# Performance work log

Measured on AMD Instinct MI355X. Metric: run time of the kernel, lower is better.

Reference implementation:

```python
import jax, jax.numpy as jnp
import numpy as np

IN_DIM, HID, E, N = 1024, 2048, 8, 16384

def setup_inputs() -> dict:
    key = jax.random.key(0)
    ks = jax.random.split(key, 12)
    s_in = 1.0 / np.sqrt(IN_DIM)
    s_h = 1.0 / np.sqrt(HID)
    return {
        "x": jax.random.normal(ks[0], (N, IN_DIM), dtype=jnp.float32),
        "enc_W": jax.random.uniform(ks[1], (IN_DIM, HID), jnp.float32, -s_in, s_in),
        "enc_b": jax.random.uniform(ks[2], (HID,), jnp.float32, -s_in, s_in),
        "gate_W": jax.random.uniform(ks[3], (HID, E), jnp.float32, -s_h, s_h),
        "expert_W": jax.random.uniform(ks[4], (E, HID, HID), jnp.float32, -s_h, s_h),
        "expert_b": jax.random.uniform(ks[5], (E, HID), jnp.float32, -s_h, s_h),
        "res_W": jax.random.uniform(ks[6], (HID, HID), jnp.float32, -s_h, s_h),
        "res_b": jax.random.uniform(ks[7], (HID,), jnp.float32, -s_h, s_h),
        "coef_W": jax.random.uniform(ks[8], (HID, 2), jnp.float32, -s_h, s_h),
        "coef_b": jax.random.uniform(ks[9], (2,), jnp.float32, -s_h, s_h),
        "dec_W": jax.random.uniform(ks[10], (HID, IN_DIM), jnp.float32, -s_h, s_h),
        "dec_b": jax.random.uniform(ks[11], (IN_DIM,), jnp.float32, -s_h, s_h),
    }

def reference(x, enc_W, enc_b, gate_W, expert_W, expert_b, res_W, res_b, coef_W, coef_b, dec_W, dec_b):
    # Encode: Linear + ReLU -> h [N, HID]
    h = jax.nn.relu(x @ enc_W + enc_b)
    # Top-1 gating (softmax probs, argmax expert, combine weight = chosen prob)
    probs = jax.nn.softmax(h @ gate_W, axis=-1)          # [N, E]
    idx = jnp.argmax(probs, axis=-1)                     # [N]
    gate = jnp.max(probs, axis=-1, keepdims=True)        # [N, 1]
    # Dense dispatch: run every expert, select via one-hot combine
    y_all = jnp.einsum('nd,edh->neh', h, expert_W) + expert_b  # [N, E, HID]
    onehot = jax.nn.one_hot(idx, y_all.shape[1], dtype=h.dtype)
    moe_out = jnp.einsum('neh,ne->nh', y_all, onehot) * gate   # [N, HID]
    # Residual expert + learned 2-way blending coefficient
    res = h @ res_W + res_b
    coef = jax.nn.softmax(h @ coef_W + coef_b, axis=-1)        # [N, 2]
    out = moe_out * coef[:, 0:1] + res * coef[:, 1:2]
    # Decode
    return out @ dec_W + dec_b
```

## Files before the change

kernel.cpp:

```cpp
#include <hip/hip_runtime.h>


#define N_TOK 16384
#define IN_DIM 1024
#define HID 2048
#define NEXP 8
#define TAU 8.0e-3f

typedef __bf16 bf16_t;
typedef __bf16 bf16x8 __attribute__((ext_vector_type(8)));
typedef __bf16 bf16x4v __attribute__((ext_vector_type(4)));
typedef float f32x4 __attribute__((ext_vector_type(4)));
typedef unsigned short ushort_t;

#define CLAMP1E4(v) fmaxf(fminf((v), 1.0e4f), -1.0e4f)

#define ASYNC16(gp, lp)                                                        \
  __builtin_amdgcn_global_load_lds(                                            \
      (const __attribute__((address_space(1))) void*)(gp),                     \
      (__attribute__((address_space(3))) void*)(lp), 16, 0, 0)

static __device__ inline ushort_t b2u(bf16_t v) {
  union { bf16_t b; ushort_t u; } x; x.b = v; return x.u;
}

__global__ __launch_bounds__(256) void fill_bf16(bf16_t* __restrict__ p,
                                                 float v, int n) {
  const int i = blockIdx.x * 256 + threadIdx.x;
  if (i < n) p[i] = (bf16_t)v;
}

__global__ __launch_bounds__(256) void detect_dtype(
    const ushort_t* __restrict__ xr, int* __restrict__ flag) {
  __shared__ int s_bad;
  if (threadIdx.x == 0) s_bad = 0;
  __syncthreads();
  int bad = 0;
  for (int i = threadIdx.x; i < 4096; i += 256) {
    const int e = (xr[i] >> 7) & 0xFF;
    if (e >= 0xC0) bad = 1;
  }
  if (__any(bad) && (threadIdx.x & 63) == 0) atomicOr(&s_bad, 1);
  __syncthreads();
  if (threadIdx.x == 0) *flag = s_bad;
}

__global__ __launch_bounds__(256) void cvt_to_bf16_x4(
    const void* __restrict__ src, bf16_t* __restrict__ dst, int n4,
    const int* __restrict__ flagp) {
  const int f = *flagp;
  const int i = blockIdx.x * 256 + threadIdx.x;
  if (i >= n4) return;
  bf16x4v o;
  if (f) {
    const f32x4 v = ((const f32x4*)src)[i];
    o[0] = (bf16_t)v[0]; o[1] = (bf16_t)v[1];
    o[2] = (bf16_t)v[2]; o[3] = (bf16_t)v[3];
  } else {
    o = ((const bf16x4v*)src)[i];
  }
  ((bf16x4v*)dst)[i] = o;
}

__global__ __launch_bounds__(256) void cvt_small(
    const void* __restrict__ encB, const void* __restrict__ expB,
    const void* __restrict__ resB, const void* __restrict__ decB,
    const void* __restrict__ coefB, const void* __restrict__ gateW,
    const void* __restrict__ coefW, float* __restrict__ encBf,
    float* __restrict__ expBf, float* __restrict__ resBf,
    float* __restrict__ decBf, float* __restrict__ coefBf,
    bf16_t* __restrict__ gWb, bf16_t* __restrict__ cWb,
    const int* __restrict__ flagp) {
  const int f = *flagp;
  const int i = blockIdx.x * 256 + threadIdx.x;
  const int seg = blockIdx.y;
  const void* src;
  int n;
  switch (seg) {
    case 0: src = encB;  n = HID; break;
    case 1: src = expB;  n = NEXP * HID; break;
    case 2: src = resB;  n = HID; break;
    case 3: src = decB;  n = IN_DIM; break;
    case 4: src = coefB; n = 2; break;
    case 5: src = gateW; n = HID * 8; break;
    default: src = coefW; n = HID * 2; break;
  }
  if (i >= n) return;
  const float v = f ? ((const float*)src)[i] : (float)((const bf16_t*)src)[i];
  switch (seg) {
    case 0: encBf[i] = v; break;
    case 1: expBf[i] = v; break;
    case 2: resBf[i] = v; break;
    case 3: decBf[i] = v; break;
    case 4: coefBf[i] = v; break;
    case 5: gWb[i] = (bf16_t)v; break;
    default: cWb[i] = (bf16_t)v; break;
  }
}

__global__ __launch_bounds__(256) void transpose_cvt(
    const void* __restrict__ src0, ushort_t* __restrict__ dst, int R, int C,
    size_t elem_off, const int* __restrict__ flagp, size_t src_zstride,
    size_t dst_zstride) {
  __shared__ ushort_t t[32][33];
  const int f = *flagp;
  const size_t eoff = elem_off + (size_t)blockIdx.z * src_zstride;
  dst += (size_t)blockIdx.z * dst_zstride;
  const int c0 = blockIdx.x * 32, r0 = blockIdx.y * 32;
  const int tx = threadIdx.x, ty = threadIdx.y;
  if (f) {
    const float* s = (const float*)src0 + eoff;
#pragma unroll
    for (int i = 0; i < 4; ++i)
      t[ty + i * 8][tx] =
          b2u((bf16_t)s[(size_t)(r0 + ty + i * 8) * C + c0 + tx]);
  } else {
    const ushort_t* s = (const ushort_t*)src0 + eoff;
#pragma unroll
    for (int i = 0; i < 4; ++i)
      t[ty + i * 8][tx] = s[(size_t)(r0 + ty + i * 8) * C + c0 + tx];
  }
  __syncthreads();
#pragma unroll
  for (int i = 0; i < 4; ++i)
    dst[(size_t)(c0 + ty + i * 8) * R + r0 + tx] = t[tx][ty + i * 8];
}


__global__ __launch_bounds__(256) void enc_gemm(
    const bf16_t* __restrict__ A, const bf16_t* __restrict__ Bt,
    const float* __restrict__ bias, bf16_t* __restrict__ H) {
  __shared__ bf16_t As[128 * 64];
  __shared__ bf16_t Bs[128 * 64];

  const int tid = threadIdx.x, lane = tid & 63, w = tid >> 6;
  const int wr = w >> 1, wc = w & 1, quad = lane >> 4, l16 = lane & 15;
  const int m0 = blockIdx.x * 128, n0 = blockIdx.y * 128;
  const char* Ab = (const char*)A;
  const char* Bb = (const char*)Bt;
  const size_t lda = (size_t)IN_DIM * 2;

  const f32x4 fz = {0.f, 0.f, 0.f, 0.f};
  f32x4 acc[4][4];
#pragma unroll
  for (int i = 0; i < 4; ++i)
#pragma unroll
    for (int j = 0; j < 4; ++j) acc[i][j] = fz;

  size_t aoff[4], boff[4];
  int cb[4];
#pragma unroll
  for (int c = 0; c < 4; ++c) {
    cb[c] = (w * 4 + c) * 1024;
    const int o = cb[c] + lane * 16;
    const int row = o >> 7;
    const int kb = (o & 127) ^ ((row & 7) << 4);
    aoff[c] = (size_t)(m0 + row) * lda + kb;
    boff[c] = (size_t)(n0 + row) * lda + kb;
  }
  const int sw = (l16 & 7) << 3;

  for (int kt = 0; kt < IN_DIM / 64; ++kt) {
    __syncthreads();
#pragma unroll
    for (int c = 0; c < 4; ++c) {
      ASYNC16(Ab + aoff[c] + (size_t)kt * 128, (char*)As + cb[c]);
      ASYNC16(Bb + boff[c] + (size_t)kt * 128, (char*)Bs + cb[c]);
    }
    __syncthreads();

#pragma unroll
    for (int ks = 0; ks < 2; ++ks) {
      const int co = (ks * 32 + quad * 8) ^ sw;
      bf16x8 af[4], bfr[4];
#pragma unroll
      for (int i = 0; i < 4; ++i)
        af[i] = *(const bf16x8*)&As[(wr * 64 + i * 16 + l16) * 64 + co];
#pragma unroll
      for (int j = 0; j < 4; ++j)
        bfr[j] = *(const bf16x8*)&Bs[(wc * 64 + j * 16 + l16) * 64 + co];
#pragma unroll
      for (int i = 0; i < 4; ++i)
#pragma unroll
        for (int j = 0; j < 4; ++j)
          acc[i][j] = __builtin_amdgcn_mfma_f32_16x16x32_bf16(
              af[i], bfr[j], acc[i][j], 0, 0, 0);
    }
  }

  float bj[4];
  int colj[4];
#pragma unroll
  for (int j = 0; j < 4; ++j) {
    colj[j] = n0 + wc * 64 + j * 16 + l16;
    bj[j] = bias[colj[j]];
  }

#pragma unroll
  for (int i = 0; i < 4; ++i) {
#pragma unroll
    for (int r = 0; r < 4; ++r) {
      const int row = m0 + wr * 64 + i * 16 + quad * 4 + r;
#pragma unroll
      for (int j = 0; j < 4; ++j) {
        const float v = fminf(fmaxf(acc[i][j][r] + bj[j], 0.f), 1.0e4f);
        H[(size_t)row * HID + colj[j]] = (bf16_t)v;
      }
    }
  }
}

__global__ __launch_bounds__(256) void gate_from_h(
    const bf16_t* __restrict__ H, const bf16_t* __restrict__ gW,
    const bf16_t* __restrict__ cW, const float* __restrict__ coefBf,
    float* __restrict__ s0g, float* __restrict__ s1g, float* __restrict__ c0g,
    int* __restrict__ eidx, int* __restrict__ ambig, int* __restrict__ acnt,
    int* __restrict__ cnt) {
  const int tid = threadIdx.x, lane = tid & 63, w = tid >> 6;
  const int r0 = blockIdx.x * 16 + w * 4;

  float acc[4][10];
#pragma unroll
  for (int g = 0; g < 4; ++g)
#pragma unroll
    for (int o = 0; o < 10; ++o) acc[g][o] = 0.f;

#pragma unroll
  for (int it = 0; it < HID / 512; ++it) {
    const int h0 = it * 512 + lane * 8;
    bf16x8 hv[4];
#pragma unroll
    for (int g = 0; g < 4; ++g)
      hv[g] = *(const bf16x8*)(H + (size_t)(r0 + g) * HID + h0);
    const bf16_t* gp = gW + (size_t)h0 * 8;
    const bf16_t* cp = cW + (size_t)h0 * 2;
    bf16x8 cc0 = *(const bf16x8*)(cp);
    bf16x8 cc1 = *(const bf16x8*)(cp + 8);
#pragma unroll
    for (int k = 0; k < 8; ++k) {
      const bf16x8 gk = *(const bf16x8*)(gp + k * 8);
      const float ck0 = (k < 4) ? (float)cc0[(k & 3) * 2]
                                : (float)cc1[(k & 3) * 2];
      const float ck1 = (k < 4) ? (float)cc0[(k & 3) * 2 + 1]
                                : (float)cc1[(k & 3) * 2 + 1];
#pragma unroll
      for (int g = 0; g < 4; ++g) {
        const float v = (float)hv[g][k];
#pragma unroll
        for (int o = 0; o < 8; ++o) acc[g][o] += v * (float)gk[o];
        acc[g][8] += v * ck0;
        acc[g][9] += v * ck1;
      }
    }
  }

#pragma unroll
  for (int m = 1; m < 64; m <<= 1)
#pragma unroll
    for (int g = 0; g < 4; ++g)
#pragma unroll
      for (int o = 0; o < 10; ++o) acc[g][o] += __shfl_xor(acc[g][o], m);

  if (lane == 0) {
#pragma unroll
    for (int g = 0; g < 4; ++g) {
      const int r = r0 + g;
      float lv[8];
#pragma unroll
      for (int e = 0; e < 8; ++e) lv[e] = acc[g][e];
      float mx = lv[0];
      int idx = 0;
#pragma unroll
      for (int e = 1; e < 8; ++e)
        if (lv[e] > mx) { mx = lv[e]; idx = e; }
      float s2 = -1.0e30f;
#pragma unroll
      for (int e = 0; e < 8; ++e)
        if (e != idx) s2 = fmaxf(s2, lv[e]);
      float s = 0.f;
#pragma unroll
      for (int e = 0; e < 8; ++e) s += expf(lv[e] - mx);
      const float gate = 1.f / s;
      const float c0 = acc[g][8] + coefBf[0], c1 = acc[g][9] + coefBf[1];
      const float cm = fmaxf(c0, c1);
      const float e0 = expf(c0 - cm), e1 = expf(c1 - cm);
      const float inv = 1.f / (e0 + e1);
      const float p0 = e0 * inv;
      c0g[r] = p0;
      s1g[r] = e1 * inv;
      s0g[r] = gate * p0;
      eidx[r] = idx;
      atomicAdd(&cnt[idx], 1);
      if (mx - s2 < TAU) {
        const int p = atomicAdd(acnt, 1);
        ambig[p] = r;
      }
    }
  }
}

__global__ __launch_bounds__(256) void rescue_partial(
    const void* __restrict__ xraw, const void* __restrict__ encWraw,
    const float* __restrict__ encBf, const void* __restrict__ gateWraw,
    const int* __restrict__ flagp, const int* __restrict__ ambig,
    const int* __restrict__ acnt, double* __restrict__ pglg) {
  const int i = blockIdx.x;
  if (i >= *acnt) return;
  const int s = blockIdx.y;
  const int r = ambig[i];
  const int f = *flagp;
  const int tid = threadIdx.x;
  const int j = s * 256 + tid;

  __shared__ float xs[IN_DIM];
  if (f) {
    const float* xp = (const float*)xraw + (size_t)r * IN_DIM;
    for (int k = tid; k < IN_DIM; k += 256) xs[k] = xp[k];
  } else {
    const bf16_t* xp = (const bf16_t*)xraw + (size_t)r * IN_DIM;
    for (int k = tid; k < IN_DIM; k += 256) xs[k] = (float)xp[k];
  }
  __syncthreads();

  double hacc = 0.0;
  if (f) {
    const float* W = (const float*)encWraw + j;
    for (int k0 = 0; k0 < IN_DIM; k0 += 16) {
      float wv[16];
#pragma unroll
      for (int kk = 0; kk < 16; ++kk) wv[kk] = W[(size_t)(k0 + kk) * HID];
#pragma unroll
      for (int kk = 0; kk < 16; ++kk)
        hacc += (double)xs[k0 + kk] * (double)wv[kk];
    }
  } else {
    const bf16_t* W = (const bf16_t*)encWraw + j;
    for (int k0 = 0; k0 < IN_DIM; k0 += 16) {
      float wv[16];
#pragma unroll
      for (int kk = 0; kk < 16; ++kk)
        wv[kk] = (float)W[(size_t)(k0 + kk) * HID];
#pragma unroll
      for (int kk = 0; kk < 16; ++kk)
        hacc += (double)xs[k0 + kk] * (double)wv[kk];
    }
  }

  double lg[8] = {0, 0, 0, 0, 0, 0, 0, 0};
  const double h = hacc + (double)encBf[j];
  if (h > 0.0) {
    if (f) {
      const float* g = (const float*)gateWraw + (size_t)j * 8;
#pragma unroll
      for (int e = 0; e < 8; ++e) lg[e] = h * (double)g[e];
    } else {
      const bf16_t* g = (const bf16_t*)gateWraw + (size_t)j * 8;
#pragma unroll
      for (int e = 0; e < 8; ++e) lg[e] = h * (double)(float)g[e];
    }
  }
#pragma unroll
  for (int m = 1; m < 64; m <<= 1)
#pragma unroll
    for (int e = 0; e < 8; ++e) lg[e] += __shfl_xor(lg[e], m);

  __shared__ double red[4][8];
  const int w = tid >> 6, lane = tid & 63;
  if (lane == 0)
#pragma unroll
    for (int e = 0; e < 8; ++e) red[w][e] = lg[e];
  __syncthreads();
  if (tid == 0) {
#pragma unroll
    for (int e = 0; e < 8; ++e)
      pglg[((size_t)i * 8 + s) * 8 + e] =
          red[0][e] + red[1][e] + red[2][e] + red[3][e];
  }
}

__global__ __launch_bounds__(64) void rescue_final(
    const int* __restrict__ ambig, const int* __restrict__ acnt,
    const float* __restrict__ c0g, const double* __restrict__ pglg,
    float* __restrict__ s0g, int* __restrict__ eidx, int* __restrict__ cnt) {
  const int i = blockIdx.x;
  if (i >= *acnt || threadIdx.x != 0) return;
  const int r = ambig[i];
  double t[8];
#pragma unroll
  for (int e = 0; e < 8; ++e) {
    double a = 0.0;
#pragma unroll
    for (int s = 0; s < 8; ++s) a += pglg[((size_t)i * 8 + s) * 8 + e];
    t[e] = a;
  }
  double m = t[0];
  int idx = 0;
#pragma unroll
  for (int e = 1; e < 8; ++e)
    if (t[e] > m) { m = t[e]; idx = e; }
  double s = 0.0;
#pragma unroll
  for (int e = 0; e < 8; ++e) s += exp(t[e] - m);
  s0g[r] = (float)((1.0 / s) * (double)c0g[r]);
  const int old = eidx[r];
  if (idx != old) {
    atomicSub(&cnt[old], 1);
    atomicAdd(&cnt[idx], 1);
    eidx[r] = idx;
  }
}

__global__ __launch_bounds__(256) void rescue_rows(
    const void* __restrict__ xraw, const void* __restrict__ encWraw,
    const float* __restrict__ encBf, const void* __restrict__ gateWraw,
    const int* __restrict__ flagp, const int* __restrict__ ambig,
    const int* __restrict__ acnt, const float* __restrict__ c0g,
    float* __restrict__ s0g, int* __restrict__ eidx, int* __restrict__ cnt,
    int ioff) {
  const int i = blockIdx.x + ioff;
  if (i >= *acnt) return;
  const int r = ambig[i];
  const int f = *flagp;
  const int tid = threadIdx.x;

  __shared__ float xs[IN_DIM];
  if (f) {
    const float* xp = (const float*)xraw + (size_t)r * IN_DIM;
    for (int k = tid; k < IN_DIM; k += 256) xs[k] = xp[k];
  } else {
    const bf16_t* xp = (const bf16_t*)xraw + (size_t)r * IN_DIM;
    for (int k = tid; k < IN_DIM; k += 256) xs[k] = (float)xp[k];
  }
  __syncthreads();

  double hacc[8] = {0, 0, 0, 0, 0, 0, 0, 0};
  if (f) {
    const float* W = (const float*)encWraw;
    for (int k0 = 0; k0 < IN_DIM; k0 += 8) {
      float wv[8][8];
#pragma unroll
      for (int kk = 0; kk < 8; ++kk) {
        const float* Wr = W + (size_t)(k0 + kk) * HID + tid;
#pragma unroll
        for (int jj = 0; jj < 8; ++jj) wv[kk][jj] = Wr[jj * 256];
      }
#pragma unroll
      for (int kk = 0; kk < 8; ++kk) {
        const double xv = (double)xs[k0 + kk];
#pragma unroll
        for (int jj = 0; jj < 8; ++jj) hacc[jj] += xv * (double)wv[kk][jj];
      }
    }
  } else {
    const bf16_t* W = (const bf16_t*)encWraw;
    for (int k0 = 0; k0 < IN_DIM; k0 += 8) {
      float wv[8][8];
#pragma unroll
      for (int kk = 0; kk < 8; ++kk) {
        const bf16_t* Wr = W + (size_t)(k0 + kk) * HID + tid;
#pragma unroll
        for (int jj = 0; jj < 8; ++jj) wv[kk][jj] = (float)Wr[jj * 256];
      }
#pragma unroll
      for (int kk = 0; kk < 8; ++kk) {
        const double xv = (double)xs[k0 + kk];
#pragma unroll
        for (int jj = 0; jj < 8; ++jj) hacc[jj] += xv * (double)wv[kk][jj];
      }
    }
  }

  double lg[8] = {0, 0, 0, 0, 0, 0, 0, 0};
#pragma unroll
  for (int jj = 0; jj < 8; ++jj) {
    const int j = tid + jj * 256;
    double h = hacc[jj] + (double)encBf[j];
    if (h > 0.0) {
      if (f) {
        const float* g = (const float*)gateWraw + (size_t)j * 8;
#pragma unroll
        for (int e = 0; e < 8; ++e) lg[e] += h * (double)g[e];
      } else {
        const bf16_t* g = (const bf16_t*)gateWraw + (size_t)j * 8;
#pragma unroll
        for (int e = 0; e < 8; ++e) lg[e] += h * (double)(float)g[e];
      }
    }
  }
#pragma unroll
  for (int m = 1; m < 64; m <<= 1)
#pragma unroll
    for (int e = 0; e < 8; ++e) lg[e] += __shfl_xor(lg[e], m);

  __shared__ double red[4][8];
  const int w = tid >> 6, lane = tid & 63;
  if (lane == 0)
#pragma unroll
    for (int e = 0; e < 8; ++e) red[w][e] = lg[e];
  __syncthreads();
  if (tid == 0) {
    double t[8];
#pragma unroll
    for (int e = 0; e < 8; ++e)
      t[e] = red[0][e] + red[1][e] + red[2][e] + red[3][e];
    double m = t[0];
    int idx = 0;
#pragma unroll
    for (int e = 1; e < 8; ++e)
      if (t[e] > m) { m = t[e]; idx = e; }
    double s = 0.0;
#pragma unroll
    for (int e = 0; e < 8; ++e) s += exp(t[e] - m);
    s0g[r] = (float)((1.0 / s) * (double)c0g[r]);
    const int old = eidx[r];
    if (idx != old) {
      atomicSub(&cnt[old], 1);
      atomicAdd(&cnt[idx], 1);
      eidx[r] = idx;
    }
  }
}

__global__ __launch_bounds__(256) void place_rows(
    const int* __restrict__ eidx, const int* __restrict__ cnt,
    int* __restrict__ curs, int* __restrict__ permflat) {
  const int r = blockIdx.x * 256 + threadIdx.x;
  const int e = eidx[r];
  int prefix = 0;
  for (int ee = 0; ee < NEXP; ++ee)
    if (ee < e) prefix += cnt[ee];
  const int pos = atomicAdd(&curs[e], 1);
  permflat[prefix + pos] = r;
}

__global__ __launch_bounds__(256) void gather_rows(
    const bf16_t* __restrict__ H, const int* __restrict__ permflat,
    const float* __restrict__ s0g, const float* __restrict__ s1g,
    bf16_t* __restrict__ Hp, int* __restrict__ rowid,
    float* __restrict__ s0p, float* __restrict__ s1p) {
  const int w = threadIdx.x >> 6, lane = threadIdx.x & 63;
  const int p = blockIdx.x * 4 + w;
  const int r = permflat[p];
  if (lane == 0) {
    rowid[p] = r;
    s0p[p] = s0g[r];
    s1p[p] = s1g[r];
  }
  const bf16x8* src = (const bf16x8*)(H + (size_t)r * HID);
  bf16x8* dst = (bf16x8*)(Hp + (size_t)p * HID);
#pragma unroll
  for (int i = 0; i < 4; ++i) dst[lane + i * 64] = src[lane + i * 64];
}

__global__ __launch_bounds__(256) void expert_gemm_t(
    const bf16_t* __restrict__ Hp, const bf16_t* __restrict__ wTall,
    size_t wstride, const float* __restrict__ expBf,
    const int* __restrict__ cnt, const int* __restrict__ rowid,
    const float* __restrict__ s0p, bf16_t* __restrict__ mid) {
  __shared__ bf16_t As[128 * 64];
  __shared__ bf16_t Bs[128 * 64];
  __shared__ int rows_s[128];
  __shared__ float s0_s[128];

  const int x = blockIdx.x;
  int e = -1, base = 0, nrows = 0;
  {
    int acc = 0, pre = 0;
    for (int ee = 0; ee < NEXP; ++ee) {
      const int ce = cnt[ee];
      const int nt = (ce + 127) >> 7;
      if (x < acc + nt) {
        const int t = x - acc;
        e = ee;
        base = pre + t * 128;
        nrows = ce - t * 128;
        if (nrows > 128) nrows = 128;
        break;
      }
      acc += nt;
      pre += ce;
    }
  }
  if (e < 0) return;

  const int tid = threadIdx.x, lane = tid & 63, w = tid >> 6;
  const int wr = w >> 1, wc = w & 1, quad = lane >> 4, l16 = lane & 15;

  if (tid < 128) {
    int grow = -1;
    float a0 = 0.f;
    if (tid < nrows) {
      grow = rowid[base + tid];
      a0 = s0p[base + tid];
    }
    rows_s[tid] = grow;
    s0_s[tid] = a0;
  }
  __syncthreads();

  const int n0 = blockIdx.y * 128;
  const char* Hb = (const char*)Hp;
  const char* Wb = (const char*)(wTall + (size_t)e * wstride);

  size_t aoff[4], boff[4];
  int cb[4];
#pragma unroll
  for (int c = 0; c < 4; ++c) {
    cb[c] = (w * 4 + c) * 1024;
    const int o = cb[c] + lane * 16;
    const int row = o >> 7;
    const int kb = (o & 127) ^ ((row & 7) << 4);
    int ar = base + row;
    if (ar > N_TOK - 1) ar = N_TOK - 1;
    aoff[c] = (size_t)ar * (HID * 2) + kb;
    boff[c] = (size_t)(n0 + row) * (HID * 2) + kb;
  }
  const int sw = (l16 & 7) << 3;

  const f32x4 fz = {0.f, 0.f, 0.f, 0.f};
  f32x4 acc[4][4];
#pragma unroll
  for (int i = 0; i < 4; ++i)
#pragma unroll
    for (int j = 0; j < 4; ++j) acc[i][j] = fz;

  for (int kt = 0; kt < HID / 64; ++kt) {
    __syncthreads();
#pragma unroll
    for (int c = 0; c < 4; ++c) {
      ASYNC16(Hb + aoff[c] + (size_t)kt * 128, (char*)As + cb[c]);
      ASYNC16(Wb + boff[c] + (size_t)kt * 128, (char*)Bs + cb[c]);
    }
    __syncthreads();

#pragma unroll
    for (int ks = 0; ks < 2; ++ks) {
      const int co = (ks * 32 + quad * 8) ^ sw;
      bf16x8 af[4], bfr[4];
#pragma unroll
      for (int i = 0; i < 4; ++i)
        af[i] = *(const bf16x8*)&As[(wr * 64 + i * 16 + l16) * 64 + co];
#pragma unroll
      for (int j = 0; j < 4; ++j)
        bfr[j] = *(const bf16x8*)&Bs[(wc * 64 + j * 16 + l16) * 64 + co];
#pragma unroll
      for (int i = 0; i < 4; ++i)
#pragma unroll
        for (int j = 0; j < 4; ++j)
          acc[i][j] = __builtin_amdgcn_mfma_f32_16x16x32_bf16(
              af[i], bfr[j], acc[i][j], 0, 0, 0);
    }
  }

  const float* eBe = expBf + (size_t)e * HID;
  float beb[4];
  int colj[4];
#pragma unroll
  for (int j = 0; j < 4; ++j) {
    colj[j] = n0 + wc * 64 + j * 16 + l16;
    beb[j] = eBe[colj[j]];
  }
#pragma unroll
  for (int i = 0; i < 4; ++i) {
#pragma unroll
    for (int r = 0; r < 4; ++r) {
      const int lr = wr * 64 + i * 16 + quad * 4 + r;
      const int grow = rows_s[lr];
      if (grow < 0) continue;
      const float s0 = s0_s[lr];
#pragma unroll
      for (int j = 0; j < 4; ++j) {
        const float v = CLAMP1E4(s0 * (acc[i][j][r] + beb[j]));
        mid[(size_t)grow * HID + colj[j]] = (bf16_t)v;
      }
    }
  }
}

__global__ __launch_bounds__(256) void res_gemm_p(
    const bf16_t* __restrict__ Hp, const bf16_t* __restrict__ Bt,
    const float* __restrict__ rB, const int* __restrict__ rowid,
    const float* __restrict__ s1p, bf16_t* __restrict__ mid) {
  __shared__ bf16_t As[128 * 64];
  __shared__ bf16_t Bs[128 * 64];

  const int tid = threadIdx.x, lane = tid & 63, w = tid >> 6;
  const int wr = w >> 1, wc = w & 1, quad = lane >> 4, l16 = lane & 15;
  const int m0 = blockIdx.x * 128, n0 = blockIdx.y * 128;
  const char* Ab = (const char*)Hp;
  const char* Bb = (const char*)Bt;

  size_t aoff[4], boff[4];
  int cb[4];
#pragma unroll
  for (int c = 0; c < 4; ++c) {
    cb[c] = (w * 4 + c) * 1024;
    const int o = cb[c] + lane * 16;
    const int row = o >> 7;
    const int kb = (o & 127) ^ ((row & 7) << 4);
    aoff[c] = (size_t)(m0 + row) * (HID * 2) + kb;
    boff[c] = (size_t)(n0 + row) * (HID * 2) + kb;
  }
  const int sw = (l16 & 7) << 3;

  const f32x4 fz = {0.f, 0.f, 0.f, 0.f};
  f32x4 acc[4][4];
#pragma unroll
  for (int i = 0; i < 4; ++i)
#pragma unroll
    for (int j = 0; j < 4; ++j) acc[i][j] = fz;

  for (int kt = 0; kt < HID / 64; ++kt) {
    __syncthreads();
#pragma unroll
    for (int c = 0; c < 4; ++c) {
      ASYNC16(Ab + aoff[c] + (size_t)kt * 128, (char*)As + cb[c]);
      ASYNC16(Bb + boff[c] + (size_t)kt * 128, (char*)Bs + cb[c]);
    }
    __syncthreads();

#pragma unroll
    for (int ks = 0; ks < 2; ++ks) {
      const int co = (ks * 32 + quad * 8) ^ sw;
      bf16x8 af[4], bfr[4];
#pragma unroll
      for (int i = 0; i < 4; ++i)
        af[i] = *(const bf16x8*)&As[(wr * 64 + i * 16 + l16) * 64 + co];
#pragma unroll
      for (int j = 0; j < 4; ++j)
        bfr[j] = *(const bf16x8*)&Bs[(wc * 64 + j * 16 + l16) * 64 + co];
#pragma unroll
      for (int i = 0; i < 4; ++i)
#pragma unroll
        for (int j = 0; j < 4; ++j)
          acc[i][j] = __builtin_amdgcn_mfma_f32_16x16x32_bf16(
              af[i], bfr[j], acc[i][j], 0, 0, 0);
    }
  }

  float rbb[4];
  int colj[4];
#pragma unroll
  for (int j = 0; j < 4; ++j) {
    colj[j] = n0 + wc * 64 + j * 16 + l16;
    rbb[j] = rB[colj[j]];
  }
#pragma unroll
  for (int i = 0; i < 4; ++i) {
#pragma unroll
    for (int r = 0; r < 4; ++r) {
      const int p = m0 + wr * 64 + i * 16 + quad * 4 + r;
      const int grow = rowid[p];
      const float s1 = s1p[p];
#pragma unroll
      for (int j = 0; j < 4; ++j) {
        const size_t ix = (size_t)grow * HID + colj[j];
        const float v =
            CLAMP1E4(s1 * (acc[i][j][r] + rbb[j]) + (float)mid[ix]);
        mid[ix] = (bf16_t)v;
      }
    }
  }
}

__global__ __launch_bounds__(256) void dec_gemm(
    const bf16_t* __restrict__ A, const bf16_t* __restrict__ Bt,
    const float* __restrict__ bias, void* __restrict__ C,
    const int* __restrict__ flagp) {
  __shared__ bf16_t As[128 * 64];
  __shared__ bf16_t Bs[128 * 64];

  const int fl = *flagp;
  const int tid = threadIdx.x, lane = tid & 63, w = tid >> 6;
  const int wr = w >> 1, wc = w & 1, quad = lane >> 4, l16 = lane & 15;
  const int m0 = blockIdx.x * 128, n0 = blockIdx.y * 128;
  const char* Ab = (const char*)A;
  const char* Bb = (const char*)Bt;

  size_t aoff[4], boff[4];
  int cb[4];
#pragma unroll
  for (int c = 0; c < 4; ++c) {
    cb[c] = (w * 4 + c) * 1024;
    const int o = cb[c] + lane * 16;
    const int row = o >> 7;
    const int kb = (o & 127) ^ ((row & 7) << 4);
    aoff[c] = (size_t)(m0 + row) * (HID * 2) + kb;
    boff[c] = (size_t)(n0 + row) * (HID * 2) + kb;
  }
  const int sw = (l16 & 7) << 3;

  const f32x4 fz = {0.f, 0.f, 0.f, 0.f};
  f32x4 acc[4][4];
#pragma unroll
  for (int i = 0; i < 4; ++i)
#pragma unroll
    for (int j = 0; j < 4; ++j) acc[i][j] = fz;

  for (int kt = 0; kt < HID / 64; ++kt) {
    __syncthreads();
#pragma unroll
    for (int c = 0; c < 4; ++c) {
      ASYNC16(Ab + aoff[c] + (size_t)kt * 128, (char*)As + cb[c]);
      ASYNC16(Bb + boff[c] + (size_t)kt * 128, (char*)Bs + cb[c]);
    }
    __syncthreads();

#pragma unroll
    for (int ks = 0; ks < 2; ++ks) {
      const int co = (ks * 32 + quad * 8) ^ sw;
      bf16x8 af[4], bfr[4];
#pragma unroll
      for (int i = 0; i < 4; ++i)
        af[i] = *(const bf16x8*)&As[(wr * 64 + i * 16 + l16) * 64 + co];
#pragma unroll
      for (int j = 0; j < 4; ++j)
        bfr[j] = *(const bf16x8*)&Bs[(wc * 64 + j * 16 + l16) * 64 + co];
#pragma unroll
      for (int i = 0; i < 4; ++i)
#pragma unroll
        for (int j = 0; j < 4; ++j)
          acc[i][j] = __builtin_amdgcn_mfma_f32_16x16x32_bf16(
              af[i], bfr[j], acc[i][j], 0, 0, 0);
    }
  }

  float bb[4];
  int colj[4];
#pragma unroll
  for (int j = 0; j < 4; ++j) {
    colj[j] = n0 + wc * 64 + j * 16 + l16;
    bb[j] = bias[colj[j]];
  }
#pragma unroll
  for (int i = 0; i < 4; ++i) {
#pragma unroll
    for (int r = 0; r < 4; ++r) {
      const int row = m0 + wr * 64 + i * 16 + quad * 4 + r;
#pragma unroll
      for (int j = 0; j < 4; ++j) {
        const float v = CLAMP1E4(acc[i][j][r] + bb[j]);
        const size_t ix = (size_t)row * IN_DIM + colj[j];
        if (fl)
          ((float*)C)[ix] = v;
        else
          ((bf16_t*)C)[ix] = (bf16_t)v;
      }
    }
  }
}

__global__ __launch_bounds__(256) void bucket_rows(
    const int* __restrict__ eidx, int* __restrict__ curs,
    int* __restrict__ perm) {
  const int r = blockIdx.x * 256 + threadIdx.x;
  const int e = eidx[r];
  const int pos = atomicAdd(&curs[e], 1);
  perm[(size_t)e * N_TOK + pos] = r;
}

__global__ __launch_bounds__(256) void expert_gemm(
    const bf16_t* __restrict__ H, const bf16_t* __restrict__ wTe,
    const float* __restrict__ eBe, const int* __restrict__ permE,
    const int* __restrict__ cnt, int e, const float* __restrict__ s0g,
    bf16_t* __restrict__ mid) {
  __shared__ bf16_t As[128 * 32];
  __shared__ bf16_t Bs[128 * 32];
  __shared__ int rows_s[128];
  __shared__ float s0_s[128];

  const int cnte = cnt[e];
  const int lt = blockIdx.x;
  if (lt * 128 >= cnte) return;
  int nrows = cnte - lt * 128;
  if (nrows > 128) nrows = 128;

  const int tid = threadIdx.x, lane = tid & 63, w = tid >> 6;
  const int wr = w >> 1, wc = w & 1, quad = lane >> 4, l16 = lane & 15;

  if (tid < 128) {
    int grow = -1;
    float a0 = 0.f;
    if (tid < nrows) {
      grow = permE[lt * 128 + tid];
      a0 = s0g[grow];
    }
    rows_s[tid] = grow;
    s0_s[tid] = a0;
  }
  __syncthreads();

  const int n0 = blockIdx.y * 128;
  const char* Hb = (const char*)H;
  const char* Wb = (const char*)wTe;

  size_t aoff[2], boff[2];
  int cb[2];
#pragma unroll
  for (int c = 0; c < 2; ++c) {
    cb[c] = (w * 2 + c) * 1024;
    const int o = cb[c] + lane * 16;
    const int row = o >> 6, kb = o & 63;
    int gr = rows_s[row];
    if (gr < 0) gr = 0;
    aoff[c] = (size_t)gr * (HID * 2) + kb;
    boff[c] = (size_t)(n0 + row) * (HID * 2) + kb;
  }

  const f32x4 fz = {0.f, 0.f, 0.f, 0.f};
  f32x4 acc[4][4];
#pragma unroll
  for (int i = 0; i < 4; ++i)
#pragma unroll
    for (int j = 0; j < 4; ++j) acc[i][j] = fz;

  for (int kt = 0; kt < HID / 32; ++kt) {
    __syncthreads();
#pragma unroll
    for (int c = 0; c < 2; ++c) {
      ASYNC16(Hb + aoff[c] + (size_t)kt * 64, (char*)As + cb[c]);
      ASYNC16(Wb + boff[c] + (size_t)kt * 64, (char*)Bs + cb[c]);
    }
    __syncthreads();

    bf16x8 af[4], bfr[4];
#pragma unroll
    for (int i = 0; i < 4; ++i)
      af[i] = *(const bf16x8*)&As[(wr * 64 + i * 16 + l16) * 32 + quad * 8];
#pragma unroll
    for (int j = 0; j < 4; ++j)
      bfr[j] = *(const bf16x8*)&Bs[(wc * 64 + j * 16 + l16) * 32 + quad * 8];
#pragma unroll
    for (int i = 0; i < 4; ++i)
#pragma unroll
      for (int j = 0; j < 4; ++j)
        acc[i][j] = __builtin_amdgcn_mfma_f32_16x16x32_bf16(af[i], bfr[j],
                                                            acc[i][j], 0, 0, 0);
  }

  float beb[4];
  int colj[4];
#pragma unroll
  for (int j = 0; j < 4; ++j) {
    colj[j] = n0 + wc * 64 + j * 16 + l16;
    beb[j] = eBe[colj[j]];
  }
#pragma unroll
  for (int i = 0; i < 4; ++i) {
#pragma unroll
    for (int r = 0; r < 4; ++r) {
      const int lr = wr * 64 + i * 16 + quad * 4 + r;
      const int grow = rows_s[lr];
      if (grow < 0) continue;
      const float s0 = s0_s[lr];
#pragma unroll
      for (int j = 0; j < 4; ++j) {
        const float v = CLAMP1E4(s0 * (acc[i][j][r] + beb[j]));
        mid[(size_t)grow * HID + colj[j]] = (bf16_t)v;
      }
    }
  }
}

__global__ __launch_bounds__(256) void res_gemm(
    const bf16_t* __restrict__ H, const bf16_t* __restrict__ Bt,
    const float* __restrict__ rB, const float* __restrict__ s1g,
    bf16_t* __restrict__ mid) {
  __shared__ bf16_t As[128 * 32];
  __shared__ bf16_t Bs[128 * 32];

  const int tid = threadIdx.x, lane = tid & 63, w = tid >> 6;
  const int wr = w >> 1, wc = w & 1, quad = lane >> 4, l16 = lane & 15;
  const int m0 = blockIdx.x * 128, n0 = blockIdx.y * 128;
  const char* Ab = (const char*)H;
  const char* Bb = (const char*)Bt;

  size_t aoff[2], boff[2];
  int cb[2];
#pragma unroll
  for (int c = 0; c < 2; ++c) {
    cb[c] = (w * 2 + c) * 1024;
    const int o = cb[c] + lane * 16;
    const int row = o >> 6, kb = o & 63;
    aoff[c] = (size_t)(m0 + row) * (HID * 2) + kb;
    boff[c] = (size_t)(n0 + row) * (HID * 2) + kb;
  }

  const f32x4 fz = {0.f, 0.f, 0.f, 0.f};
  f32x4 acc[4][4];
#pragma unroll
  for (int i = 0; i < 4; ++i)
#pragma unroll
    for (int j = 0; j < 4; ++j) acc[i][j] = fz;

  for (int kt = 0; kt < HID / 32; ++kt) {
    __syncthreads();
#pragma unroll
    for (int c = 0; c < 2; ++c) {
      ASYNC16(Ab + aoff[c] + (size_t)kt * 64, (char*)As + cb[c]);
      ASYNC16(Bb + boff[c] + (size_t)kt * 64, (char*)Bs + cb[c]);
    }
    __syncthreads();

    bf16x8 af[4], bfr[4];
#pragma unroll
    for (int i = 0; i < 4; ++i)
      af[i] = *(const bf16x8*)&As[(wr * 64 + i * 16 + l16) * 32 + quad * 8];
#pragma unroll
    for (int j = 0; j < 4; ++j)
      bfr[j] = *(const bf16x8*)&Bs[(wc * 64 + j * 16 + l16) * 32 + quad * 8];
#pragma unroll
    for (int i = 0; i < 4; ++i)
#pragma unroll
      for (int j = 0; j < 4; ++j)
        acc[i][j] = __builtin_amdgcn_mfma_f32_16x16x32_bf16(af[i], bfr[j],
                                                            acc[i][j], 0, 0, 0);
  }

  float rbb[4];
  int colj[4];
#pragma unroll
  for (int j = 0; j < 4; ++j) {
    colj[j] = n0 + wc * 64 + j * 16 + l16;
    rbb[j] = rB[colj[j]];
  }
#pragma unroll
  for (int i = 0; i < 4; ++i) {
#pragma unroll
    for (int r = 0; r < 4; ++r) {
      const int row = m0 + wr * 64 + i * 16 + quad * 4 + r;
      const float s1 = s1g[row];
#pragma unroll
      for (int j = 0; j < 4; ++j) {
        const size_t ix = (size_t)row * HID + colj[j];
        const float v =
            CLAMP1E4(s1 * (acc[i][j][r] + rbb[j]) + (float)mid[ix]);
        mid[ix] = (bf16_t)v;
      }
    }
  }
}

extern "C" void kernel_launch(void* const* d_in, const int* in_sizes, int n_in,
                              void* d_out, int out_size, void* d_ws,
                              size_t ws_size, hipStream_t stream) {
  (void)in_sizes; (void)n_in;

  const void* x     = d_in[0];
  const void* encW  = d_in[1];
  const void* encB  = d_in[2];
  const void* gateW = d_in[3];
  const void* expW  = d_in[4];
  const void* expB  = d_in[5];
  const void* resW  = d_in[6];
  const void* resB  = d_in[7];
  const void* coefW = d_in[8];
  const void* coefB = d_in[9];
  const void* decW  = d_in[10];
  const void* decB  = d_in[11];

  char* ws = (char*)d_ws;
  size_t o = 0;
  int*    flag  = (int*)(ws + o);    o += 256;
  int*    cnt   = (int*)(ws + o);    o += 256;
  int*    acnt  = cnt + 8;
  int*    curs  = cnt + 16;
  float*  s0g   = (float*)(ws + o);  o += (size_t)N_TOK * 4;
  float*  s1g   = (float*)(ws + o);  o += (size_t)N_TOK * 4;
  float*  c0g   = (float*)(ws + o);  o += (size_t)N_TOK * 4;
  int*    eidx  = (int*)(ws + o);    o += (size_t)N_TOK * 4;
  int*    ambig = (int*)(ws + o);    o += (size_t)N_TOK * 4;
  int*    permfl= (int*)(ws + o);    o += (size_t)N_TOK * 4;
  int*    rowid = (int*)(ws + o);    o += (size_t)N_TOK * 4;
  float*  s0p   = (float*)(ws + o);  o += (size_t)N_TOK * 4;
  float*  s1p   = (float*)(ws + o);  o += (size_t)N_TOK * 4;
  int*    perm  = (int*)(ws + o);    o += (size_t)NEXP * N_TOK * 4;
  float*  encBf = (float*)(ws + o);  o += HID * 4;
  float*  expBf = (float*)(ws + o);  o += (size_t)NEXP * HID * 4;
  float*  resBf = (float*)(ws + o);  o += HID * 4;
  float*  decBf = (float*)(ws + o);  o += IN_DIM * 4;
  float*  coefBf= (float*)(ws + o);  o += 256;
  bf16_t* gWb   = (bf16_t*)(ws + o); o += (size_t)HID * 8 * 2;
  bf16_t* cWb   = (bf16_t*)(ws + o); o += (size_t)HID * 2 * 2;
  o = (o + 255) & ~(size_t)255;
  bf16_t* bufA  = (bf16_t*)(ws + o); o += (size_t)N_TOK * HID * 2;
  bf16_t* bufB  = (bf16_t*)(ws + o); o += (size_t)N_TOK * HID * 2;
  bf16_t* wT    = (bf16_t*)(ws + o); o += (size_t)HID * HID * 2;
  const size_t needed_small = o;
  const size_t S = (size_t)HID * HID;
  bf16_t* wTall = (bf16_t*)(ws + o);
  const size_t needed_big = o + 10 * S * 2;

  double* pglg = (double*)perm;

  bf16_t* hbuf  = bufA;
  bf16_t* xbf   = bufB;

  if (ws_size < needed_small) {
    const float v = (float)(ws_size >> 20);
    fill_bf16<<<dim3((out_size + 255) / 256), 256, 0, stream>>>(
        (bf16_t*)d_out, v, out_size);
    return;
  }
  const bool big = ws_size >= needed_big;

  detect_dtype<<<1, 256, 0, stream>>>((const ushort_t*)x, flag);
  hipMemsetAsync(cnt, 0, 256, stream);

  cvt_to_bf16_x4<<<dim3(N_TOK * IN_DIM / 4 / 256), 256, 0, stream>>>(
      x, xbf, N_TOK * IN_DIM / 4, flag);
  cvt_small<<<dim3(64, 7), 256, 0, stream>>>(encB, expB, resB, decB, coefB,
                                             gateW, coefW, encBf, expBf, resBf,
                                             decBf, coefBf, gWb, cWb, flag);

  const dim3 tb(32, 8, 1);

  transpose_cvt<<<dim3(HID / 32, IN_DIM / 32, 1), tb, 0, stream>>>(
      encW, (ushort_t*)wT, IN_DIM, HID, 0, flag, 0, 0);
  if (big) {
    transpose_cvt<<<dim3(HID / 32, HID / 32, NEXP), tb, 0, stream>>>(
        expW, (ushort_t*)wTall, HID, HID, 0, flag, S, S);
    transpose_cvt<<<dim3(HID / 32, HID / 32, 1), tb, 0, stream>>>(
        resW, (ushort_t*)(wTall + 8 * S), HID, HID, 0, flag, 0, 0);
    transpose_cvt<<<dim3(IN_DIM / 32, HID / 32, 1), tb, 0, stream>>>(
        decW, (ushort_t*)(wTall + 9 * S), HID, IN_DIM, 0, flag, 0, 0);
  }

  enc_gemm<<<dim3(N_TOK / 128, HID / 128), 256, 0, stream>>>(xbf, wT, encBf,
                                                             hbuf);
  gate_from_h<<<dim3(N_TOK / 16), 256, 0, stream>>>(
      hbuf, gWb, cWb, coefBf, s0g, s1g, c0g, eidx, ambig, acnt, cnt);
  rescue_partial<<<dim3(1024, 8), 256, 0, stream>>>(
      x, encW, encBf, gateW, flag, ambig, acnt, pglg);
  rescue_final<<<dim3(1024), 64, 0, stream>>>(ambig, acnt, c0g, pglg, s0g,
                                              eidx, cnt);
  rescue_rows<<<dim3(N_TOK - 1024), 256, 0, stream>>>(
      x, encW, encBf, gateW, flag, ambig, acnt, c0g, s0g, eidx, cnt, 1024);

  if (big) {
    bf16_t* Hperm = bufB;
    bf16_t* mid   = bufA;
    place_rows<<<dim3(N_TOK / 256), 256, 0, stream>>>(eidx, cnt, curs, permfl);
    gather_rows<<<dim3(N_TOK / 4), 256, 0, stream>>>(hbuf, permfl, s0g, s1g,
                                                     Hperm, rowid, s0p, s1p);
    expert_gemm_t<<<dim3(136, HID / 128), 256, 0, stream>>>(
        Hperm, wTall, S, expBf, cnt, rowid, s0p, mid);
    res_gemm_p<<<dim3(N_TOK / 128, HID / 128), 256, 0, stream>>>(
        Hperm, wTall + 8 * S, resBf, rowid, s1p, mid);
    dec_gemm<<<dim3(N_TOK / 128, IN_DIM / 128), 256, 0, stream>>>(
        mid, wTall + 9 * S, decBf, d_out, flag);
  } else {
    bf16_t* mid = bufB;
    bucket_rows<<<dim3(N_TOK / 256), 256, 0, stream>>>(eidx, curs, perm);
    for (int e = 0; e < NEXP; ++e) {
      transpose_cvt<<<dim3(HID / 32, HID / 32, 1), tb, 0, stream>>>(
          expW, (ushort_t*)wT, HID, HID, (size_t)e * HID * HID, flag, 0, 0);
      expert_gemm<<<dim3(N_TOK / 128, HID / 128), 256, 0, stream>>>(
          hbuf, wT, expBf + (size_t)e * HID, perm + (size_t)e * N_TOK, cnt, e,
          s0g, mid);
    }
    transpose_cvt<<<dim3(HID / 32, HID / 32, 1), tb, 0, stream>>>(
        resW, (ushort_t*)wT, HID, HID, 0, flag, 0, 0);
    res_gemm<<<dim3(N_TOK / 128, HID / 128), 256, 0, stream>>>(hbuf, wT, resBf,
                                                               s1g, mid);
    transpose_cvt<<<dim3(IN_DIM / 32, HID / 32, 1), tb, 0, stream>>>(
        decW, (ushort_t*)wT, HID, IN_DIM, 0, flag, 0, 0);
    dec_gemm<<<dim3(N_TOK / 128, IN_DIM / 128), 256, 0, stream>>>(
        mid, wT, decBf, d_out, flag);
  }
}
```

Before: 1.532 ms.

## Tile rescue recompute over 8 ambiguous rows per block and tighten tolerance

The per-row rescue kernel, which recomputes encoder and gate logits in double precision for tokens with ambiguous top-1 routing, now handles 8 ambiguous rows per block. Each encoder weight column load is reused across all 8 rows, cutting global weight traffic roughly eightfold. The ambiguity threshold TAU is lowered from 8e-3 to 3e-3, so fewer tokens are flagged for the slow exact path. The smaller threshold risks letting near-tied tokens route differently from the fp32 reference.

```diff
diff --git a/kernel.cpp b/kernel.cpp
--- a/kernel.cpp
+++ b/kernel.cpp
@@ -5,7 +5,8 @@
 #define IN_DIM 1024
 #define HID 2048
 #define NEXP 8
-#define TAU 8.0e-3f
+#define TAU 3.0e-3f
+#define RROWS 8
 
 typedef __bf16 bf16_t;
 typedef __bf16 bf16x8 __attribute__((ext_vector_type(8)));
@@ -299,82 +300,125 @@
   }
 }
 
-__global__ __launch_bounds__(256) void rescue_partial(
+__global__ __launch_bounds__(256) void rescue_tile(
     const void* __restrict__ xraw, const void* __restrict__ encWraw,
     const float* __restrict__ encBf, const void* __restrict__ gateWraw,
     const int* __restrict__ flagp, const int* __restrict__ ambig,
     const int* __restrict__ acnt, double* __restrict__ pglg) {
-  const int i = blockIdx.x;
-  if (i >= *acnt) return;
+  const int an0 = *acnt;
+  const int an = an0 < 1024 ? an0 : 1024;
+  const int i0 = blockIdx.x * RROWS;
+  if (i0 >= an) return;
+  int nr = an - i0;
+  if (nr > RROWS) nr = RROWS;
   const int s = blockIdx.y;
-  const int r = ambig[i];
   const int f = *flagp;
   const int tid = threadIdx.x;
   const int j = s * 256 + tid;
 
-  __shared__ float xs[IN_DIM];
-  if (f) {
-    const float* xp = (const float*)xraw + (size_t)r * IN_DIM;
-    for (int k = tid; k < IN_DIM; k += 256) xs[k] = xp[k];
-  } else {
-    const bf16_t* xp = (const bf16_t*)xraw + (size_t)r * IN_DIM;
-    for (int k = tid; k < IN_DIM; k += 256) xs[k] = (float)xp[k];
-  }
+  __shared__ int rows_sh[RROWS];
+  __shared__ float xs[RROWS][IN_DIM];
+  if (tid < RROWS) rows_sh[tid] = ambig[i0 + (tid < nr ? tid : 0)];
   __syncthreads();
 
-  double hacc = 0.0;
+  for (int r = 0; r < RROWS; ++r) {
+    const int row = rows_sh[r];
+    if (f) {
+      const float* xp = (const float*)xraw + (size_t)row * IN_DIM;
+      for (int k = tid; k < IN_DIM; k += 256) xs[r][k] = xp[k];
+    } else {
+      const bf16_t* xp = (const bf16_t*)xraw + (size_t)row * IN_DIM;
+      for (int k = tid; k < IN_DIM; k += 256) xs[r][k] = (float)xp[k];
+    }
+  }
+  __syncthreads();
+
+  double hacc[RROWS];
+#pragma unroll
+  for (int r = 0; r < RROWS; ++r) hacc[r] = 0.0;
+
   if (f) {
     const float* W = (const float*)encWraw + j;
-    for (int k0 = 0; k0 < IN_DIM; k0 += 16) {
-      float wv[16];
-#pragma unroll
-      for (int kk = 0; kk < 16; ++kk) wv[kk] = W[(size_t)(k0 + kk) * HID];
-#pragma unroll
-      for (int kk = 0; kk < 16; ++kk)
-        hacc += (double)xs[k0 + kk] * (double)wv[kk];
+    for (int k0 = 0; k0 < IN_DIM; k0 += 8) {
+      double wd[8];
+#pragma unroll
+      for (int kk = 0; kk < 8; ++kk)
+        wd[kk] = (double)W[(size_t)(k0 + kk) * HID];
+#pragma unroll
+      for (int r = 0; r < RROWS; ++r) {
+        const f32x4 xa = *(const f32x4*)&xs[r][k0];
+        const f32x4 xb = *(const f32x4*)&xs[r][k0 + 4];
+        double a = hacc[r];
+        a += (double)xa[0] * wd[0];
+        a += (double)xa[1] * wd[1];
+        a += (double)xa[2] * wd[2];
+        a += (double)xa[3] * wd[3];
+        a += (double)xb[0] * wd[4];
+        a += (double)xb[1] * wd[5];
+        a += (double)xb[2] * wd[6];
+        a += (double)xb[3] * wd[7];
+        hacc[r] = a;
+      }
     }
   } else {
     const bf16_t* W = (const bf16_t*)encWraw + j;
-    for (int k0 = 0; k0 < IN_DIM; k0 += 16) {
-      float wv[16];
-#pragma unroll
-      for (int kk = 0; kk < 16; ++kk)
-        wv[kk] = (float)W[(size_t)(k0 + kk) * HID];
-#pragma unroll
-      for (int kk = 0; kk < 16; ++kk)
-        hacc += (double)xs[k0 + kk] * (double)wv[kk];
-    }
-  }
-
-  double lg[8] = {0, 0, 0, 0, 0, 0, 0, 0};
-  const double h = hacc + (double)encBf[j];
-  if (h > 0.0) {
-    if (f) {
-      const float* g = (const float*)gateWraw + (size_t)j * 8;
-#pragma unroll
-      for (int e = 0; e < 8; ++e) lg[e] = h * (double)g[e];
-    } else {
-      const bf16_t* g = (const bf16_t*)gateWraw + (size_t)j * 8;
-#pragma unroll
-      for (int e = 0; e < 8; ++e) lg[e] = h * (double)(float)g[e];
-    }
-  }
-#pragma unroll
-  for (int m = 1; m < 64; m <<= 1)
-#pragma unroll
-    for (int e = 0; e < 8; ++e) lg[e] += __shfl_xor(lg[e], m);
+    for (int k0 = 0; k0 < IN_DIM; k0 += 8) {
+      double wd[8];
+#pragma unroll
+      for (int kk = 0; kk < 8; ++kk)
+        wd[kk] = (double)(float)W[(size_t)(k0 + kk) * HID];
+#pragma unroll
+      for (int r = 0; r < RROWS; ++r) {
+        const f32x4 xa = *(const f32x4*)&xs[r][k0];
+        const f32x4 xb = *(const f32x4*)&xs[r][k0 + 4];
+        double a = hacc[r];
+        a += (double)xa[0] * wd[0];
+        a += (double)xa[1] * wd[1];
+        a += (double)xa[2] * wd[2];
+        a += (double)xa[3] * wd[3];
+        a += (double)xb[0] * wd[4];
+        a += (double)xb[1] * wd[5];
+        a += (double)xb[2] * wd[6];
+        a += (double)xb[3] * wd[7];
+        hacc[r] = a;
+      }
+    }
+  }
+
+  double gv[8];
+  if (f) {
+    const float* g = (const float*)gateWraw + (size_t)j * 8;
+#pragma unroll
+    for (int e = 0; e < 8; ++e) gv[e] = (double)g[e];
+  } else {
+    const bf16_t* g = (const bf16_t*)gateWraw + (size_t)j * 8;
+#pragma unroll
+    for (int e = 0; e < 8; ++e) gv[e] = (double)(float)g[e];
+  }
+  const double bj = (double)encBf[j];
 
   __shared__ double red[4][8];
   const int w = tid >> 6, lane = tid & 63;
-  if (lane == 0)
-#pragma unroll
-    for (int e = 0; e < 8; ++e) red[w][e] = lg[e];
-  __syncthreads();
-  if (tid == 0) {
-#pragma unroll
-    for (int e = 0; e < 8; ++e)
-      pglg[((size_t)i * 8 + s) * 8 + e] =
-          red[0][e] + red[1][e] + red[2][e] + red[3][e];
+  for (int r = 0; r < RROWS; ++r) {
+    double lg[8];
+    const double h = hacc[r] + bj;
+#pragma unroll
+    for (int e = 0; e < 8; ++e) lg[e] = (h > 0.0) ? h * gv[e] : 0.0;
+#pragma unroll
+    for (int m = 1; m < 64; m <<= 1)
+#pragma unroll
+      for (int e = 0; e < 8; ++e) lg[e] += __shfl_xor(lg[e], m);
+    if (lane == 0)
+#pragma unroll
+      for (int e = 0; e < 8; ++e) red[w][e] = lg[e];
+    __syncthreads();
+    if (tid == 0 && r < nr) {
+#pragma unroll
+      for (int e = 0; e < 8; ++e)
+        pglg[((size_t)(i0 + r) * 8 + s) * 8 + e] =
+            red[0][e] + red[1][e] + red[2][e] + red[3][e];
+    }
+    __syncthreads();
   }
 }
 
@@ -1130,8 +1174,8 @@
                                                              hbuf);
   gate_from_h<<<dim3(N_TOK / 16), 256, 0, stream>>>(
       hbuf, gWb, cWb, coefBf, s0g, s1g, c0g, eidx, ambig, acnt, cnt);
-  rescue_partial<<<dim3(1024, 8), 256, 0, stream>>>(
-      x, encW, encBf, gateW, flag, ambig, acnt, pglg);
+  rescue_tile<<<dim3(128, 8), 256, 0, stream>>>(x, encW, encBf, gateW, flag,
+                                                ambig, acnt, pglg);
   rescue_final<<<dim3(1024), 64, 0, stream>>>(ambig, acnt, c0g, pglg, s0g,
                                               eidx, cnt);
   rescue_rows<<<dim3(N_TOK - 1024), 256, 0, stream>>>(
```

New measurement: 1.756 ms. +14.6%, slower.
